# Performance work log

Measured on AMD Instinct MI355X. Metric: run time of the kernel, lower is better.

Reference implementation:

```python
import jax, jax.numpy as jnp
import numpy as np

GRID = 16
N = GRID * GRID          # num_nodes = 256
D = 64                   # embed_dim
SPARSITY = 0.8
BATCH = 2048


def setup_inputs() -> dict:
    key = jax.random.key(0)
    ks = jax.random.split(key, 11)
    s1 = 1.0 / np.sqrt(D)          # fan_in of per-node Linears
    s2 = 1.0 / np.sqrt(N * D)      # fan_in of global_pool first Linear
    x = jax.random.normal(ks[0], (BATCH, N * D), dtype=jnp.float32)
    adj_param = jax.random.normal(ks[1], (N, N), dtype=jnp.float32) * 0.1
    W1 = jax.random.uniform(ks[2], (N, D, D), minval=-s1, maxval=s1, dtype=jnp.float32)
    b1 = jax.random.uniform(ks[3], (N, D), minval=-s1, maxval=s1, dtype=jnp.float32)
    W2 = jax.random.uniform(ks[4], (N, D, D), minval=-s1, maxval=s1, dtype=jnp.float32)
    b2 = jax.random.uniform(ks[5], (N, D), minval=-s1, maxval=s1, dtype=jnp.float32)
    gpW1 = jax.random.uniform(ks[6], (N * D, D), minval=-s2, maxval=s2, dtype=jnp.float32)
    gpb1 = jax.random.uniform(ks[7], (D,), minval=-s2, maxval=s2, dtype=jnp.float32)
    gpW2 = jax.random.uniform(ks[8], (D, D // 2), minval=-s1, maxval=s1, dtype=jnp.float32)
    gpb2 = jax.random.uniform(ks[9], (D // 2,), minval=-s1, maxval=s1, dtype=jnp.float32)
    return {"x": x, "adj_param": adj_param, "W1": W1, "b1": b1, "W2": W2, "b2": b2,
            "gpW1": gpW1, "gpb1": gpb1, "gpW2": gpW2, "gpb2": gpb2}


def _adjacency(adj_param):
    adj = jax.nn.sigmoid(adj_param)
    # threshold = sorted(flat adj)[int(sparsity * N*N)], then hard-threshold, then zero diagonal
    thr = jnp.sort(adj.reshape(-1))[int(SPARSITY * N * N)]
    adj = adj * (adj > thr)
    return adj * (1.0 - jnp.eye(N, dtype=adj.dtype))


def reference(x, adj_param, W1, b1, W2, b2, gpW1, gpb1, gpW2, gpb2):
    B = x.shape[0]
    adj = _adjacency(adj_param)
    xn = x.reshape(B, N, D)                                    # [B, N, D]
    # per-node distinct MLP == grouped GEMM with weights [N, D, D]
    h = jax.nn.relu(jnp.einsum('bnd,nde->bne', xn, W1) + b1)   # [B, N, D]
    node = jnp.einsum('bnd,nde->bne', h, W2) + b2              # [B, N, D]
    # adjacency-weighted neighbor sum: mixed[b,i] = sum_j adj[i,j] * node[b,j]
    mixed = jnp.einsum('ij,bjd->bid', adj, node)               # [B, N, D]
    final = 0.5 * mixed + 0.5 * node                           # residual mix
    g = jax.nn.relu(final.reshape(B, N * D) @ gpW1 + gpb1)     # [B, D]
    out = g @ gpW2 + gpb2                                      # [B, D//2]
    return out, adj
```

## Files before the change

### kernel.cpp

```cpp
#include <hip/hip_runtime.h>
#include <math.h>

typedef unsigned int uint;
typedef unsigned short ushort;
typedef short short8 __attribute__((ext_vector_type(8)));
typedef float f32x4 __attribute__((ext_vector_type(4)));

#define B_ 2048
#define N_ 256
#define D_ 64
#define ND_ 16384
#define NN_ 65536
#define KIDX_ 52428u
#define NGROUPS 32

#define WS_W1T    ((size_t)0)
#define WS_W2T    ((size_t)2*1024*1024)
#define WS_EFF    ((size_t)4*1024*1024)
#define WS_GPARTS ((size_t)8*1024*1024)
#define WS_SCAL   ((size_t)24*1024*1024)

__device__ __forceinline__ ushort f2bf(float f) {
    uint u = __float_as_uint(f);
    u += 0x7fffu + ((u >> 16) & 1u);
    return (ushort)(u >> 16);
}
__device__ __forceinline__ float bf2f(ushort u) { return __uint_as_float(((uint)u) << 16); }

__device__ __forceinline__ float sigmoid_exact(float a) {
    float t = (float)exp(-(double)a);
    return 1.0f / (1.0f + t);
}

__device__ __forceinline__ uint f2key(uint bits) {
    return bits ^ ((bits & 0x80000000u) ? 0xFFFFFFFFu : 0x80000000u);
}

__device__ __forceinline__ int wfrag_off(int e, int k) {
    return ((((e >> 4) * 2 + (k >> 5)) * 4 + ((k >> 3) & 3)) * 16 + (e & 15)) * 8 + (k & 7);
}

__device__ __forceinline__ int afrag_off(int jl, int i) {
    return (((((jl >> 4) * 8 + (i >> 5)) * 4 + ((i >> 3) & 3)) * 16) + (jl & 15)) * 8 + (i & 7);
}

__global__ __launch_bounds__(1024) void k_cvt_radix(const float* __restrict__ W1,
                                                    const float* __restrict__ W2,
                                                    const float* __restrict__ adj_param,
                                                    ushort* __restrict__ W1f,
                                                    ushort* __restrict__ W2f,
                                                    uint* __restrict__ scal) {
    __shared__ uint SH[16402] __attribute__((aligned(16)));
    int bid = blockIdx.x, tid = threadIdx.x;

    if (bid != 0) {
        int q = tid >> 8, t = tid & 255;
        int m = (bid - 1) * 4 + q;
        ushort* P = (ushort*)SH + q * 4096;
        const float* src = (m < 256) ? W1 + (size_t)m * 4096 : W2 + (size_t)(m - 256) * 4096;
#pragma unroll
        for (int i = 0; i < 16; i++) {
            int idx = i * 256 + t;
            int k = idx >> 6, e = idx & 63;
            P[wfrag_off(e, k)] = f2bf(src[idx]);
        }
        __syncthreads();
        ushort* dst = (m < 256) ? W1f + (size_t)m * 4096 : W2f + (size_t)(m - 256) * 4096;
#pragma unroll
        for (int i = 0; i < 2; i++)
            ((uint4*)dst)[i * 256 + t] = ((const uint4*)P)[i * 256 + t];
        return;
    }

    uint* hist = SH;
    uint* wsum = SH + 16384;
    uint* bc   = SH + 16400;
    const uint4* pv = (const uint4*)adj_param;
    uint rank = KIDX_;
    uint pref = 0u;
#pragma unroll 1
    for (int lvl = 0; lvl < 3; lvl++) {
        int nb  = (lvl == 2) ? 1024 : 2048;
        int sh  = (lvl == 0) ? 21 : (lvl == 1) ? 10 : 0;
        uint pm = (lvl == 0) ? 0u : (lvl == 1) ? 0xFFE00000u : 0xFFFFFC00u;
        for (int i = tid; i < nb * 8; i += 1024) hist[i] = 0u;
        __syncthreads();
        int sub = tid & 7;
#pragma unroll 1
        for (int i = 0; i < 16; i++) {
            uint4 v = pv[i * 1024 + tid];
#define H_(B) { uint k_ = f2key(B); if (((k_ ^ pref) & pm) == 0u) \
                atomicAdd(&hist[(((k_ >> sh) & (uint)(nb - 1)) << 3) + sub], 1u); }
            H_(v.x) H_(v.y) H_(v.z) H_(v.w)
#undef H_
        }
        __syncthreads();
        int bpt = nb >> 10;
        int b0 = tid * bpt;
        uint c0 = 0, c1 = 0;
#pragma unroll
        for (int k = 0; k < 8; k++) c0 += hist[(b0 << 3) + k];
        if (bpt == 2) {
#pragma unroll
            for (int k = 0; k < 8; k++) c1 += hist[((b0 + 1) << 3) + k];
        }
        uint s = c0 + c1;
        uint sc = s;
#pragma unroll
        for (int o = 1; o < 64; o <<= 1) {
            uint t2 = __shfl_up(sc, o, 64);
            if ((tid & 63) >= o) sc += t2;
        }
        if ((tid & 63) == 63) wsum[tid >> 6] = sc;
        __syncthreads();
        uint base = 0;
        for (int w = 0; w < (tid >> 6); w++) base += wsum[w];
        uint c = base + sc - s;
        if (rank >= c && rank < c + c0) { bc[0] = (uint)b0; bc[1] = rank - c; }
        c += c0;
        if (bpt == 2 && rank >= c && rank < c + c1) { bc[0] = (uint)(b0 + 1); bc[1] = rank - c; }
        __syncthreads();
        pref |= bc[0] << sh;
        rank = bc[1];
        __syncthreads();
    }
    if (tid == 0) {
        uint key = pref;
        uint bits = (key & 0x80000000u) ? (key ^ 0x80000000u) : ~key;
        scal[0] = __float_as_uint(sigmoid_exact(__uint_as_float(bits)));
    }
}

__global__ __launch_bounds__(256) void k_threff(const float* __restrict__ adj_param,
                                                const uint* __restrict__ scal,
                                                const float* __restrict__ gpW1,
                                                float* __restrict__ adj_out,
                                                ushort* __restrict__ effF) {
    __shared__ ushort adjS[16384] __attribute__((aligned(16)));
    __shared__ ushort Bf[16384] __attribute__((aligned(16)));
    int d = blockIdx.x, jt = blockIdx.y, tid = threadIdx.x;
    float thr = __uint_as_float(scal[0]);

    {
        int jl = tid & 63;
        int jglob = jt * 64 + jl;
        int wrow = tid >> 6;
#pragma unroll 1
        for (int i = 0; i < 16; i++) {
            float p[4];
#pragma unroll
            for (int u = 0; u < 4; u++)
                p[u] = adj_param[(size_t)((i * 4 + u) * 4 + wrow) * 256 + jglob];
#pragma unroll
            for (int u = 0; u < 4; u++) {
                int ir = (i * 4 + u) * 4 + wrow;
                float s = sigmoid_exact(p[u]);
                float v = (s > thr && ir != jglob) ? s : 0.0f;
                adjS[afrag_off(jl, ir)] = f2bf(v);
                if (d == 0) adj_out[(size_t)ir * 256 + jglob] = v;
            }
        }
    }
#pragma unroll
    for (int t = 0; t < 16; t++) {
        int idx = t * 256 + tid;
        int i = idx >> 4;
        int f4 = idx & 15;
        float4 v = *(const float4*)(gpW1 + ((size_t)i * 64 + d) * 64 + f4 * 4);
        int slab = i >> 6, il = i & 63, e0 = f4 * 4;
        Bf[slab * 4096 + wfrag_off(e0 + 0, il)] = f2bf(v.x);
        Bf[slab * 4096 + wfrag_off(e0 + 1, il)] = f2bf(v.y);
        Bf[slab * 4096 + wfrag_off(e0 + 2, il)] = f2bf(v.z);
        Bf[slab * 4096 + wfrag_off(e0 + 3, il)] = f2bf(v.w);
    }
    __syncthreads();
    int wid = tid >> 6, lane = tid & 63, quad = lane >> 4, l16 = lane & 15;
    f32x4 acc[4];
#pragma unroll
    for (int nt = 0; nt < 4; nt++) acc[nt] = (f32x4){0.f, 0.f, 0.f, 0.f};
#pragma unroll
    for (int ks8 = 0; ks8 < 8; ks8++) {
        short8 af = *(const short8*)&adjS[((((wid * 8 + ks8) * 4 + quad) * 16 + l16)) * 8];
        int slab = ks8 >> 1, ks = ks8 & 1;
#pragma unroll
        for (int nt = 0; nt < 4; nt++) {
            short8 bf = *(const short8*)&Bf[slab * 4096 + (((nt * 2 + ks) * 4 + quad) * 16 + l16) * 8];
            acc[nt] = __builtin_amdgcn_mfma_f32_16x16x32_bf16(af, bf, acc[nt], 0, 0, 0);
        }
    }
#pragma unroll
    for (int nt = 0; nt < 4; nt++) {
        int e = nt * 16 + l16;
#pragma unroll
        for (int r = 0; r < 4; r++) {
            int j = jt * 64 + wid * 16 + quad * 4 + r;
            float w = gpW1[((size_t)j * 64 + d) * 64 + e];
            float eff = 0.5f * (acc[nt][r] + w);
            effF[(size_t)j * 4096 + wfrag_off(e, d)] = f2bf(eff);
        }
    }
}

__global__ __launch_bounds__(512, 4) void k_fused(const float* __restrict__ x,
                                                  const ushort* __restrict__ W1f,
                                                  const ushort* __restrict__ W2f,
                                                  const ushort* __restrict__ effF,
                                                  const float* __restrict__ b1,
                                                  const float* __restrict__ b2,
                                                  float* __restrict__ gparts) {
    __shared__ ushort Wf1[4096] __attribute__((aligned(16)));
    __shared__ ushort Wf2[4096] __attribute__((aligned(16)));
    __shared__ ushort Ef[4096] __attribute__((aligned(16)));
    __shared__ ushort St[8][16 * 72];
    __shared__ float Bs[2][8][64];
    int tid = threadIdx.x;
    int g = blockIdx.x, bt = blockIdx.y;
    int wid = tid >> 6, lane = tid & 63, quad = lane >> 4, l16 = lane & 15;
    int rbase = bt * 128 + wid * 16;
    ushort* Sw = &St[wid][0];
    const float* xrow = x + (size_t)(rbase + l16) * ND_ + quad * 8;

    ((float*)Bs[0])[tid] = b1[(size_t)g * 512 + tid];
    ((float*)Bs[1])[tid] = b2[(size_t)g * 512 + tid];

    int n0 = g * 8;
    uint4 w1a = ((const uint4*)(W1f + (size_t)n0 * 4096))[tid];
    uint4 w2a = ((const uint4*)(W2f + (size_t)n0 * 4096))[tid];
    uint4 ea  = ((const uint4*)(effF + (size_t)n0 * 4096))[tid];
    float4 xr0, xr1, xr2, xr3;
    {
        const float* xp = xrow + (size_t)n0 * 64;
        xr0 = *(const float4*)(xp);
        xr1 = *(const float4*)(xp + 4);
        xr2 = *(const float4*)(xp + 32);
        xr3 = *(const float4*)(xp + 36);
    }
    ((uint4*)Wf1)[tid] = w1a;
    ((uint4*)Wf2)[tid] = w2a;
    ((uint4*)Ef)[tid]  = ea;

    f32x4 accg[4];
#pragma unroll
    for (int nt = 0; nt < 4; nt++) accg[nt] = (f32x4){0.f, 0.f, 0.f, 0.f};

    __syncthreads();

#pragma unroll 1
    for (int nl = 0; nl < 8; nl++) {
        short8 fa0, fa1;
        {
            short8 a;
            a[0] = (short)f2bf(xr0.x); a[1] = (short)f2bf(xr0.y);
            a[2] = (short)f2bf(xr0.z); a[3] = (short)f2bf(xr0.w);
            a[4] = (short)f2bf(xr1.x); a[5] = (short)f2bf(xr1.y);
            a[6] = (short)f2bf(xr1.z); a[7] = (short)f2bf(xr1.w);
            fa0 = a;
            short8 b;
            b[0] = (short)f2bf(xr2.x); b[1] = (short)f2bf(xr2.y);
            b[2] = (short)f2bf(xr2.z); b[3] = (short)f2bf(xr2.w);
            b[4] = (short)f2bf(xr3.x); b[5] = (short)f2bf(xr3.y);
            b[6] = (short)f2bf(xr3.z); b[7] = (short)f2bf(xr3.w);
            fa1 = b;
        }

        if (nl < 7) {
            int nn = g * 8 + nl + 1;
            w1a = ((const uint4*)(W1f + (size_t)nn * 4096))[tid];
            w2a = ((const uint4*)(W2f + (size_t)nn * 4096))[tid];
            ea  = ((const uint4*)(effF + (size_t)nn * 4096))[tid];
            const float* xp = xrow + (size_t)nn * 64;
            xr0 = *(const float4*)(xp);
            xr1 = *(const float4*)(xp + 4);
            xr2 = *(const float4*)(xp + 32);
            xr3 = *(const float4*)(xp + 36);
        }

        float bias1[4], bias2[4];
#pragma unroll
        for (int nt = 0; nt < 4; nt++) {
            bias1[nt] = Bs[0][nl][nt * 16 + l16];
            bias2[nt] = Bs[1][nl][nt * 16 + l16];
        }

        f32x4 acc[4];
#pragma unroll
        for (int nt = 0; nt < 4; nt++) acc[nt] = (f32x4){0.f, 0.f, 0.f, 0.f};
#pragma unroll
        for (int nt = 0; nt < 4; nt++) {
            short8 bf = *(const short8*)&Wf1[(((nt * 2 + 0) * 4 + quad) * 16 + l16) * 8];
            acc[nt] = __builtin_amdgcn_mfma_f32_16x16x32_bf16(fa0, bf, acc[nt], 0, 0, 0);
        }
#pragma unroll
        for (int nt = 0; nt < 4; nt++) {
            short8 bf = *(const short8*)&Wf1[(((nt * 2 + 1) * 4 + quad) * 16 + l16) * 8];
            acc[nt] = __builtin_amdgcn_mfma_f32_16x16x32_bf16(fa1, bf, acc[nt], 0, 0, 0);
        }
#pragma unroll
        for (int nt = 0; nt < 4; nt++)
#pragma unroll
            for (int r = 0; r < 4; r++) {
                float h = fmaxf(acc[nt][r] + bias1[nt], 0.0f);
                Sw[(quad * 4 + r) * 72 + nt * 16 + l16] = f2bf(h);
            }
        f32x4 acc2[4];
#pragma unroll
        for (int nt = 0; nt < 4; nt++) acc2[nt] = (f32x4){0.f, 0.f, 0.f, 0.f};
#pragma unroll
        for (int ks = 0; ks < 2; ks++) {
            short8 a2 = *(const short8*)&Sw[l16 * 72 + ks * 32 + quad * 8];
#pragma unroll
            for (int nt = 0; nt < 4; nt++) {
                short8 bf = *(const short8*)&Wf2[(((nt * 2 + ks) * 4 + quad) * 16 + l16) * 8];
                acc2[nt] = __builtin_amdgcn_mfma_f32_16x16x32_bf16(a2, bf, acc2[nt], 0, 0, 0);
            }
        }
#pragma unroll
        for (int nt = 0; nt < 4; nt++)
#pragma unroll
            for (int r = 0; r < 4; r++) {
                float v = acc2[nt][r] + bias2[nt];
                Sw[(quad * 4 + r) * 72 + nt * 16 + l16] = f2bf(v);
            }
#pragma unroll
        for (int ks = 0; ks < 2; ks++) {
            short8 a3 = *(const short8*)&Sw[l16 * 72 + ks * 32 + quad * 8];
#pragma unroll
            for (int nt = 0; nt < 4; nt++) {
                short8 bf = *(const short8*)&Ef[(((nt * 2 + ks) * 4 + quad) * 16 + l16) * 8];
                accg[nt] = __builtin_amdgcn_mfma_f32_16x16x32_bf16(a3, bf, accg[nt], 0, 0, 0);
            }
        }

        if (nl < 7) {
            __syncthreads();
            ((uint4*)Wf1)[tid] = w1a;
            ((uint4*)Wf2)[tid] = w2a;
            ((uint4*)Ef)[tid]  = ea;
            __syncthreads();
        }
    }

    float* gp = gparts + ((size_t)g * B_ + bt * 128) * 64;
#pragma unroll
    for (int nt = 0; nt < 4; nt++)
#pragma unroll
        for (int r = 0; r < 4; r++) {
            int b_loc = wid * 16 + quad * 4 + r;
            int e = nt * 16 + l16;
            gp[b_loc * 64 + e] = accg[nt][r];
        }
}

__global__ __launch_bounds__(256) void k_gp2(const float* __restrict__ gparts,
                                             const float* __restrict__ gpb1,
                                             const float* __restrict__ gpW2,
                                             const float* __restrict__ gpb2,
                                             float* __restrict__ out) {
    __shared__ float gs[4][64];
    int b0 = blockIdx.x * 4, tid = threadIdx.x;
    int r = tid >> 6, e = tid & 63;
    float s = gpb1[e];
#pragma unroll
    for (int p = 0; p < NGROUPS; p++)
        s += gparts[((size_t)p * B_ + b0 + r) * 64 + e];
    gs[r][e] = fmaxf(s, 0.0f);
    __syncthreads();
    if (tid < 128) {
        int rr = tid >> 5, o = tid & 31;
        float a = gpb2[o];
#pragma unroll 8
        for (int k2 = 0; k2 < 64; k2++) a += gs[rr][k2] * gpW2[k2 * 32 + o];
        out[(size_t)(b0 + rr) * 32 + o] = a;
    }
}

extern "C" void kernel_launch(void* const* d_in, const int* in_sizes, int n_in,
                              void* d_out, int out_size, void* d_ws, size_t ws_size,
                              hipStream_t stream) {
    const float* x = (const float*)d_in[0];
    const float* adj_param = (const float*)d_in[1];
    const float* W1 = (const float*)d_in[2];
    const float* b1 = (const float*)d_in[3];
    const float* W2 = (const float*)d_in[4];
    const float* b2 = (const float*)d_in[5];
    const float* gpW1 = (const float*)d_in[6];
    const float* gpb1 = (const float*)d_in[7];
    const float* gpW2 = (const float*)d_in[8];
    const float* gpb2 = (const float*)d_in[9];

    float* out = (float*)d_out;
    float* adj_out = (float*)d_out + NN_;

    char* ws = (char*)d_ws;
    ushort* W1f = (ushort*)(ws + WS_W1T);
    ushort* W2f = (ushort*)(ws + WS_W2T);
    ushort* effF = (ushort*)(ws + WS_EFF);
    float* gparts = (float*)(ws + WS_GPARTS);
    uint* scal = (uint*)(ws + WS_SCAL);

    k_cvt_radix<<<129, 1024, 0, stream>>>(W1, W2, adj_param, W1f, W2f, scal);
    k_threff<<<dim3(64, 4), 256, 0, stream>>>(adj_param, scal, gpW1, adj_out, effF);
    k_fused<<<dim3(NGROUPS, 16), 512, 0, stream>>>(x, W1f, W2f, effF, b1, b2, gparts);
    k_gp2<<<512, 256, 0, stream>>>(gparts, gpb1, gpW2, gpb2, out);
}
```

Measured before the change: 270.2 us.

## Compute thresholded adjacency once in radix block; prefetch x two nodes ahead

```diff
diff --git a/kernel.cpp b/kernel.cpp
--- a/kernel.cpp
+++ b/kernel.cpp
@@ -18,7 +18,7 @@
 #define WS_W2T    ((size_t)2*1024*1024)
 #define WS_EFF    ((size_t)4*1024*1024)
 #define WS_GPARTS ((size_t)8*1024*1024)
-#define WS_SCAL   ((size_t)24*1024*1024)
+#define WS_ADJF   ((size_t)24*1024*1024)
 
 __device__ __forceinline__ ushort f2bf(float f) {
     uint u = __float_as_uint(f);
@@ -38,10 +38,6 @@
 
 __device__ __forceinline__ int wfrag_off(int e, int k) {
     return ((((e >> 4) * 2 + (k >> 5)) * 4 + ((k >> 3) & 3)) * 16 + (e & 15)) * 8 + (k & 7);
-}
-
-__device__ __forceinline__ int afrag_off(int jl, int i) {
-    return (((((jl >> 4) * 8 + (i >> 5)) * 4 + ((i >> 3) & 3)) * 16) + (jl & 15)) * 8 + (i & 7);
 }
 
 __global__ __launch_bounds__(1024) void k_cvt_radix(const float* __restrict__ W1,
@@ -49,7 +45,8 @@
                                                     const float* __restrict__ adj_param,
                                                     ushort* __restrict__ W1f,
                                                     ushort* __restrict__ W2f,
-                                                    uint* __restrict__ scal) {
+                                                    float* __restrict__ adj_out,
+                                                    ushort* __restrict__ adjF) {
     __shared__ uint SH[16402] __attribute__((aligned(16)));
     int bid = blockIdx.x, tid = threadIdx.x;
 
@@ -124,43 +121,36 @@
         rank = bc[1];
         __syncthreads();
     }
-    if (tid == 0) {
+
+    float thr;
+    {
         uint key = pref;
         uint bits = (key & 0x80000000u) ? (key ^ 0x80000000u) : ~key;
-        scal[0] = __float_as_uint(sigmoid_exact(__uint_as_float(bits)));
-    }
-}
-
-__global__ __launch_bounds__(256) void k_threff(const float* __restrict__ adj_param,
-                                                const uint* __restrict__ scal,
-                                                const float* __restrict__ gpW1,
-                                                float* __restrict__ adj_out,
-                                                ushort* __restrict__ effF) {
-    __shared__ ushort adjS[16384] __attribute__((aligned(16)));
+        thr = sigmoid_exact(__uint_as_float(bits));
+    }
+#pragma unroll 1
+    for (int ib = 0; ib < 16; ib++) {
+        uint4 v = pv[ib * 1024 + tid];
+        int i0 = (ib * 1024 + tid) * 4;
+#pragma unroll
+        for (int c4 = 0; c4 < 4; c4++) {
+            uint bits = (c4 == 0) ? v.x : (c4 == 1) ? v.y : (c4 == 2) ? v.z : v.w;
+            int i = i0 + c4;
+            float s = sigmoid_exact(__uint_as_float(bits));
+            int r = i >> 8, c = i & 255;
+            float val = (s > thr && r != c) ? s : 0.0f;
+            adj_out[i] = val;
+            uint chunk = ((((uint)(c >> 4) * 8u + (uint)(r >> 5)) * 4u + (uint)((r >> 3) & 3)) * 16u + (uint)(c & 15));
+            adjF[chunk * 8u + (uint)(r & 7)] = f2bf(val);
+        }
+    }
+}
+
+__global__ __launch_bounds__(256) void k_eff(const ushort* __restrict__ adjF,
+                                             const float* __restrict__ gpW1,
+                                             ushort* __restrict__ effF) {
     __shared__ ushort Bf[16384] __attribute__((aligned(16)));
     int d = blockIdx.x, jt = blockIdx.y, tid = threadIdx.x;
-    float thr = __uint_as_float(scal[0]);
-
-    {
-        int jl = tid & 63;
-        int jglob = jt * 64 + jl;
-        int wrow = tid >> 6;
-#pragma unroll 1
-        for (int i = 0; i < 16; i++) {
-            float p[4];
-#pragma unroll
-            for (int u = 0; u < 4; u++)
-                p[u] = adj_param[(size_t)((i * 4 + u) * 4 + wrow) * 256 + jglob];
-#pragma unroll
-            for (int u = 0; u < 4; u++) {
-                int ir = (i * 4 + u) * 4 + wrow;
-                float s = sigmoid_exact(p[u]);
-                float v = (s > thr && ir != jglob) ? s : 0.0f;
-                adjS[afrag_off(jl, ir)] = f2bf(v);
-                if (d == 0) adj_out[(size_t)ir * 256 + jglob] = v;
-            }
-        }
-    }
 #pragma unroll
     for (int t = 0; t < 16; t++) {
         int idx = t * 256 + tid;
@@ -180,7 +170,7 @@
     for (int nt = 0; nt < 4; nt++) acc[nt] = (f32x4){0.f, 0.f, 0.f, 0.f};
 #pragma unroll
     for (int ks8 = 0; ks8 < 8; ks8++) {
-        short8 af = *(const short8*)&adjS[((((wid * 8 + ks8) * 4 + quad) * 16 + l16)) * 8];
+        short8 af = *(const short8*)&adjF[(size_t)(((((jt * 4 + wid) * 8 + ks8) * 4 + quad) * 16 + l16)) * 8];
         int slab = ks8 >> 1, ks = ks8 & 1;
 #pragma unroll
         for (int nt = 0; nt < 4; nt++) {
@@ -198,6 +188,110 @@
             float eff = 0.5f * (acc[nt][r] + w);
             effF[(size_t)j * 4096 + wfrag_off(e, d)] = f2bf(eff);
         }
+    }
+}
+
+__device__ __forceinline__ void node_step(int nl, int g, int tid, int quad, int l16,
+                                          const float* xrow,
+                                          const ushort* __restrict__ W1f,
+                                          const ushort* __restrict__ W2f,
+                                          const ushort* __restrict__ effF,
+                                          ushort* Wf1, ushort* Wf2, ushort* Ef,
+                                          ushort* Sw, const float* b1s, const float* b2s,
+                                          float4& x0, float4& x1, float4& x2, float4& x3,
+                                          uint4& w1a, uint4& w2a, uint4& ea,
+                                          f32x4* accg) {
+    short8 fa0, fa1;
+    {
+        short8 a;
+        a[0] = (short)f2bf(x0.x); a[1] = (short)f2bf(x0.y);
+        a[2] = (short)f2bf(x0.z); a[3] = (short)f2bf(x0.w);
+        a[4] = (short)f2bf(x1.x); a[5] = (short)f2bf(x1.y);
+        a[6] = (short)f2bf(x1.z); a[7] = (short)f2bf(x1.w);
+        fa0 = a;
+        short8 b;
+        b[0] = (short)f2bf(x2.x); b[1] = (short)f2bf(x2.y);
+        b[2] = (short)f2bf(x2.z); b[3] = (short)f2bf(x2.w);
+        b[4] = (short)f2bf(x3.x); b[5] = (short)f2bf(x3.y);
+        b[6] = (short)f2bf(x3.z); b[7] = (short)f2bf(x3.w);
+        fa1 = b;
+    }
+    if (nl < 7) {
+        int nn = g * 8 + nl + 1;
+        w1a = ((const uint4*)(W1f + (size_t)nn * 4096))[tid];
+        w2a = ((const uint4*)(W2f + (size_t)nn * 4096))[tid];
+        ea  = ((const uint4*)(effF + (size_t)nn * 4096))[tid];
+    }
+    if (nl < 6) {
+        const float* xp = xrow + (size_t)(g * 8 + nl + 2) * 64;
+        x0 = *(const float4*)(xp);
+        x1 = *(const float4*)(xp + 4);
+        x2 = *(const float4*)(xp + 32);
+        x3 = *(const float4*)(xp + 36);
+    }
+
+    float bias1[4], bias2[4];
+#pragma unroll
+    for (int nt = 0; nt < 4; nt++) {
+        bias1[nt] = b1s[nl * 64 + nt * 16 + l16];
+        bias2[nt] = b2s[nl * 64 + nt * 16 + l16];
+    }
+
+    f32x4 acc[4];
+#pragma unroll
+    for (int nt = 0; nt < 4; nt++) acc[nt] = (f32x4){0.f, 0.f, 0.f, 0.f};
+#pragma unroll
+    for (int nt = 0; nt < 4; nt++) {
+        short8 bf = *(const short8*)&Wf1[(((nt * 2 + 0) * 4 + quad) * 16 + l16) * 8];
+        acc[nt] = __builtin_amdgcn_mfma_f32_16x16x32_bf16(fa0, bf, acc[nt], 0, 0, 0);
+    }
+#pragma unroll
+    for (int nt = 0; nt < 4; nt++) {
+        short8 bf = *(const short8*)&Wf1[(((nt * 2 + 1) * 4 + quad) * 16 + l16) * 8];
+        acc[nt] = __builtin_amdgcn_mfma_f32_16x16x32_bf16(fa1, bf, acc[nt], 0, 0, 0);
+    }
+#pragma unroll
+    for (int nt = 0; nt < 4; nt++)
+#pragma unroll
+        for (int r = 0; r < 4; r++) {
+            float h = fmaxf(acc[nt][r] + bias1[nt], 0.0f);
+            Sw[(quad * 4 + r) * 72 + nt * 16 + l16] = f2bf(h);
+        }
+    f32x4 acc2[4];
+#pragma unroll
+    for (int nt = 0; nt < 4; nt++) acc2[nt] = (f32x4){0.f, 0.f, 0.f, 0.f};
+#pragma unroll
+    for (int ks = 0; ks < 2; ks++) {
+        short8 a2 = *(const short8*)&Sw[l16 * 72 + ks * 32 + quad * 8];
+#pragma unroll
+        for (int nt = 0; nt < 4; nt++) {
+            short8 bf = *(const short8*)&Wf2[(((nt * 2 + ks) * 4 + quad) * 16 + l16) * 8];
+            acc2[nt] = __builtin_amdgcn_mfma_f32_16x16x32_bf16(a2, bf, acc2[nt], 0, 0, 0);
+        }
+    }
+#pragma unroll
+    for (int nt = 0; nt < 4; nt++)
+#pragma unroll
+        for (int r = 0; r < 4; r++) {
+            float v = acc2[nt][r] + bias2[nt];
+            Sw[(quad * 4 + r) * 72 + nt * 16 + l16] = f2bf(v);
+        }
+#pragma unroll
+    for (int ks = 0; ks < 2; ks++) {
+        short8 a3 = *(const short8*)&Sw[l16 * 72 + ks * 32 + quad * 8];
+#pragma unroll
+        for (int nt = 0; nt < 4; nt++) {
+            short8 bf = *(const short8*)&Ef[(((nt * 2 + ks) * 4 + quad) * 16 + l16) * 8];
+            accg[nt] = __builtin_amdgcn_mfma_f32_16x16x32_bf16(a3, bf, accg[nt], 0, 0, 0);
+        }
+    }
+
+    if (nl < 7) {
+        __syncthreads();
+        ((uint4*)Wf1)[tid] = w1a;
+        ((uint4*)Wf2)[tid] = w2a;
+        ((uint4*)Ef)[tid]  = ea;
+        __syncthreads();
     }
 }
 
@@ -227,13 +321,18 @@
     uint4 w1a = ((const uint4*)(W1f + (size_t)n0 * 4096))[tid];
     uint4 w2a = ((const uint4*)(W2f + (size_t)n0 * 4096))[tid];
     uint4 ea  = ((const uint4*)(effF + (size_t)n0 * 4096))[tid];
-    float4 xr0, xr1, xr2, xr3;
+    float4 xa0, xa1, xa2, xa3, xb0, xb1, xb2, xb3;
     {
         const float* xp = xrow + (size_t)n0 * 64;
-        xr0 = *(const float4*)(xp);
-        xr1 = *(const float4*)(xp + 4);
-        xr2 = *(const float4*)(xp + 32);
-        xr3 = *(const float4*)(xp + 36);
+        xa0 = *(const float4*)(xp);
+        xa1 = *(const float4*)(xp + 4);
+        xa2 = *(const float4*)(xp + 32);
+        xa3 = *(const float4*)(xp + 36);
+        const float* xq = xrow + (size_t)(n0 + 1) * 64;
+        xb0 = *(const float4*)(xq);
+        xb1 = *(const float4*)(xq + 4);
+        xb2 = *(const float4*)(xq + 32);
+        xb3 = *(const float4*)(xq + 36);
     }
     ((uint4*)Wf1)[tid] = w1a;
     ((uint4*)Wf2)[tid] = w2a;
@@ -245,99 +344,14 @@
 
     __syncthreads();
 
+    const float* b1s = &Bs[0][0][0];
+    const float* b2s = &Bs[1][0][0];
 #pragma unroll 1
-    for (int nl = 0; nl < 8; nl++) {
-        short8 fa0, fa1;
-        {
-            short8 a;
-            a[0] = (short)f2bf(xr0.x); a[1] = (short)f2bf(xr0.y);
-            a[2] = (short)f2bf(xr0.z); a[3] = (short)f2bf(xr0.w);
-            a[4] = (short)f2bf(xr1.x); a[5] = (short)f2bf(xr1.y);
-            a[6] = (short)f2bf(xr1.z); a[7] = (short)f2bf(xr1.w);
-            fa0 = a;
-            short8 b;
-            b[0] = (short)f2bf(xr2.x); b[1] = (short)f2bf(xr2.y);
-            b[2] = (short)f2bf(xr2.z); b[3] = (short)f2bf(xr2.w);
-            b[4] = (short)f2bf(xr3.x); b[5] = (short)f2bf(xr3.y);
-            b[6] = (short)f2bf(xr3.z); b[7] = (short)f2bf(xr3.w);
-            fa1 = b;
-        }
-
-        if (nl < 7) {
-            int nn = g * 8 + nl + 1;
-            w1a = ((const uint4*)(W1f + (size_t)nn * 4096))[tid];
-            w2a = ((const uint4*)(W2f + (size_t)nn * 4096))[tid];
-            ea  = ((const uint4*)(effF + (size_t)nn * 4096))[tid];
-            const float* xp = xrow + (size_t)nn * 64;
-            xr0 = *(const float4*)(xp);
-            xr1 = *(const float4*)(xp + 4);
-            xr2 = *(const float4*)(xp + 32);
-            xr3 = *(const float4*)(xp + 36);
-        }
-
-        float bias1[4], bias2[4];
-#pragma unroll
-        for (int nt = 0; nt < 4; nt++) {
-            bias1[nt] = Bs[0][nl][nt * 16 + l16];
-            bias2[nt] = Bs[1][nl][nt * 16 + l16];
-        }
-
-        f32x4 acc[4];
-#pragma unroll
-        for (int nt = 0; nt < 4; nt++) acc[nt] = (f32x4){0.f, 0.f, 0.f, 0.f};
-#pragma unroll
-        for (int nt = 0; nt < 4; nt++) {
-            short8 bf = *(const short8*)&Wf1[(((nt * 2 + 0) * 4 + quad) * 16 + l16) * 8];
-            acc[nt] = __builtin_amdgcn_mfma_f32_16x16x32_bf16(fa0, bf, acc[nt], 0, 0, 0);
-        }
-#pragma unroll
-        for (int nt = 0; nt < 4; nt++) {
-            short8 bf = *(const short8*)&Wf1[(((nt * 2 + 1) * 4 + quad) * 16 + l16) * 8];
-            acc[nt] = __builtin_amdgcn_mfma_f32_16x16x32_bf16(fa1, bf, acc[nt], 0, 0, 0);
-        }
-#pragma unroll
-        for (int nt = 0; nt < 4; nt++)
-#pragma unroll
-            for (int r = 0; r < 4; r++) {
-                float h = fmaxf(acc[nt][r] + bias1[nt], 0.0f);
-                Sw[(quad * 4 + r) * 72 + nt * 16 + l16] = f2bf(h);
-            }
-        f32x4 acc2[4];
-#pragma unroll
-        for (int nt = 0; nt < 4; nt++) acc2[nt] = (f32x4){0.f, 0.f, 0.f, 0.f};
-#pragma unroll
-        for (int ks = 0; ks < 2; ks++) {
-            short8 a2 = *(const short8*)&Sw[l16 * 72 + ks * 32 + quad * 8];
-#pragma unroll
-            for (int nt = 0; nt < 4; nt++) {
-                short8 bf = *(const short8*)&Wf2[(((nt * 2 + ks) * 4 + quad) * 16 + l16) * 8];
-                acc2[nt] = __builtin_amdgcn_mfma_f32_16x16x32_bf16(a2, bf, acc2[nt], 0, 0, 0);
-            }
-        }
-#pragma unroll
-        for (int nt = 0; nt < 4; nt++)
-#pragma unroll
-            for (int r = 0; r < 4; r++) {
-                float v = acc2[nt][r] + bias2[nt];
-                Sw[(quad * 4 + r) * 72 + nt * 16 + l16] = f2bf(v);
-            }
-#pragma unroll
-        for (int ks = 0; ks < 2; ks++) {
-            short8 a3 = *(const short8*)&Sw[l16 * 72 + ks * 32 + quad * 8];
-#pragma unroll
-            for (int nt = 0; nt < 4; nt++) {
-                short8 bf = *(const short8*)&Ef[(((nt * 2 + ks) * 4 + quad) * 16 + l16) * 8];
-                accg[nt] = __builtin_amdgcn_mfma_f32_16x16x32_bf16(a3, bf, accg[nt], 0, 0, 0);
-            }
-        }
-
-        if (nl < 7) {
-            __syncthreads();
-            ((uint4*)Wf1)[tid] = w1a;
-            ((uint4*)Wf2)[tid] = w2a;
-            ((uint4*)Ef)[tid]  = ea;
-            __syncthreads();
-        }
+    for (int np = 0; np < 4; np++) {
+        node_step(np * 2,     g, tid, quad, l16, xrow, W1f, W2f, effF,
+                  Wf1, Wf2, Ef, Sw, b1s, b2s, xa0, xa1, xa2, xa3, w1a, w2a, ea, accg);
+        node_step(np * 2 + 1, g, tid, quad, l16, xrow, W1f, W2f, effF,
+                  Wf1, Wf2, Ef, Sw, b1s, b2s, xb0, xb1, xb2, xb3, w1a, w2a, ea, accg);
     }
 
     float* gp = gparts + ((size_t)g * B_ + bt * 128) * 64;
@@ -396,10 +410,10 @@
     ushort* W2f = (ushort*)(ws + WS_W2T);
     ushort* effF = (ushort*)(ws + WS_EFF);
     float* gparts = (float*)(ws + WS_GPARTS);
-    uint* scal = (uint*)(ws + WS_SCAL);
-
-    k_cvt_radix<<<129, 1024, 0, stream>>>(W1, W2, adj_param, W1f, W2f, scal);
-    k_threff<<<dim3(64, 4), 256, 0, stream>>>(adj_param, scal, gpW1, adj_out, effF);
+    ushort* adjF = (ushort*)(ws + WS_ADJF);
+
+    k_cvt_radix<<<129, 1024, 0, stream>>>(W1, W2, adj_param, W1f, W2f, adj_out, adjF);
+    k_eff<<<dim3(64, 4), 256, 0, stream>>>(adjF, gpW1, effF);
     k_fused<<<dim3(NGROUPS, 16), 512, 0, stream>>>(x, W1f, W2f, effF, b1, b2, gparts);
     k_gp2<<<512, 256, 0, stream>>>(gparts, gpb1, gpW2, gpb2, out);
 }
```

Result: slower. 298.4 us (+10.5%).
